# Kernel optimization log

Measured on AMD Instinct MI355X. Metric: run time of the kernel, lower is better.

The kernel has to match this reference:

```python
import jax, jax.numpy as jnp
import numpy as np

EMBED = 768
NHEAD = 12
HEAD_DIM = EMBED // NHEAD


def setup_inputs() -> dict:
    key = jax.random.key(0)
    ks = jax.random.split(key, 6)
    bs, seq = 4, 2048
    x = jax.random.normal(ks[0], (bs, seq, EMBED), dtype=jnp.float32)
    attmask = jax.random.randint(ks[1], (bs, seq), 0, 2, dtype=jnp.int32)
    # xavier-uniform-ish init for weights
    lim_qkv = float(np.sqrt(6.0 / (EMBED + 3 * EMBED)))
    W_qkv = jax.random.uniform(ks[2], (EMBED, 3 * EMBED), minval=-lim_qkv, maxval=lim_qkv, dtype=jnp.float32)
    b_qkv = jnp.zeros((3 * EMBED,), dtype=jnp.float32)
    lim_p = float(np.sqrt(6.0 / (EMBED + EMBED)))
    W_proj = jax.random.uniform(ks[3], (EMBED, EMBED), minval=-lim_p, maxval=lim_p, dtype=jnp.float32)
    b_proj = jnp.zeros((EMBED,), dtype=jnp.float32)
    return {"x": x, "attmask": attmask, "W_qkv": W_qkv, "b_qkv": b_qkv, "W_proj": W_proj, "b_proj": b_proj}


def reference(x, attmask, W_qkv, b_qkv, W_proj, b_proj):
    bs, seq, embed = x.shape
    qkv = x @ W_qkv + b_qkv                     # [bs, seq, 3*embed]
    q, k, v = jnp.split(qkv, 3, axis=-1)
    def to_heads(t):
        return t.reshape(bs, seq, NHEAD, HEAD_DIM).transpose(0, 2, 1, 3)  # [bs, h, seq, d]
    q, k, v = to_heads(q), to_heads(k), to_heads(v)
    scale = 1.0 / np.sqrt(HEAD_DIM).astype(np.float32)
    scores = jnp.einsum('bhqd,bhkd->bhqk', q, k) * scale  # [bs, h, seq, seq]
    mask = (attmask == 0)[:, None, None, :]               # [bs,1,1,seq]
    scores = jnp.where(mask, jnp.asarray(-10000.0, scores.dtype), scores)
    att = jax.nn.softmax(scores, axis=-1)                  # dropout p=0.0 -> identity
    y = jnp.einsum('bhqk,bhkd->bhqd', att, v)              # [bs, h, seq, d]
    y = y.transpose(0, 2, 1, 3).reshape(bs, seq, embed)
    return y @ W_proj + b_proj
```

## Files before the change

### kernel.cpp

```cpp
#include <hip/hip_runtime.h>

typedef unsigned short u16;
typedef unsigned int u32;
typedef __attribute__((ext_vector_type(8))) short short8;
typedef __attribute__((ext_vector_type(4))) short s16x4;
typedef __attribute__((ext_vector_type(4))) float f32x4;

__device__ __forceinline__ float b2f(u16 u) {
    union { u32 i; float f; } v; v.i = ((u32)u) << 16; return v.f;
}
__device__ __forceinline__ u16 f2b(float f) {
    union { u32 i; float f; } v; v.f = f;
    u32 u = v.i;
    return (u16)((u + 0x7FFFu + ((u >> 16) & 1u)) >> 16);
}
__device__ __forceinline__ f32x4 zero4() {
    f32x4 v; v[0] = 0.f; v[1] = 0.f; v[2] = 0.f; v[3] = 0.f; return v;
}
__device__ __forceinline__ u32 cvtpk(float lo, float hi) {
    u32 d;
    asm("v_cvt_pk_bf16_f32 %0, %1, %2" : "=v"(d) : "v"(lo), "v"(hi));
    return d;
}
__device__ __forceinline__ float fexp2(float x) {
#if __has_builtin(__builtin_amdgcn_exp2f)
    return __builtin_amdgcn_exp2f(x);
#else
    return __expf(x * 0.6931471805599453f);
#endif
}
__device__ __forceinline__ void gload16(const u16* g, u16* l) {
    __builtin_amdgcn_global_load_lds(
        (const __attribute__((address_space(1))) u32*)g,
        (__attribute__((address_space(3))) u32*)l, 16, 0, 0);
}

__global__ void convert_kernel(const float* __restrict__ src, u16* __restrict__ dst,
                               int n8) {
    const int stride = gridDim.x * blockDim.x;
    for (int i = blockIdx.x * blockDim.x + threadIdx.x; i < n8; i += stride) {
        const float* s = src + (size_t)i * 8;
        float4 a = ((const float4*)s)[0];
        float4 b = ((const float4*)s)[1];
        short8 o;
        o[0] = (short)f2b(a.x); o[1] = (short)f2b(a.y);
        o[2] = (short)f2b(a.z); o[3] = (short)f2b(a.w);
        o[4] = (short)f2b(b.x); o[5] = (short)f2b(b.y);
        o[6] = (short)f2b(b.z); o[7] = (short)f2b(b.w);
        ((short8*)dst)[i] = o;
    }
}

__global__ void tconvert_kernel(const float* __restrict__ src, u16* __restrict__ dst,
                                int K, int N) {
    __shared__ u16 T[64][72];
    const int n0 = blockIdx.x * 64, k0 = blockIdx.y * 64;
    const int tid = threadIdx.x;
    const int r = tid >> 3, cq = tid & 7;
#pragma unroll
    for (int half = 0; half < 2; half++) {
        const int k = k0 + half * 32 + r;
        const float* s = &src[(size_t)k * N + n0 + cq * 8];
        const float4 f0 = ((const float4*)s)[0];
        const float4 f1 = ((const float4*)s)[1];
        T[cq * 8 + 0][half * 32 + r] = f2b(f0.x);
        T[cq * 8 + 1][half * 32 + r] = f2b(f0.y);
        T[cq * 8 + 2][half * 32 + r] = f2b(f0.z);
        T[cq * 8 + 3][half * 32 + r] = f2b(f0.w);
        T[cq * 8 + 4][half * 32 + r] = f2b(f1.x);
        T[cq * 8 + 5][half * 32 + r] = f2b(f1.y);
        T[cq * 8 + 6][half * 32 + r] = f2b(f1.z);
        T[cq * 8 + 7][half * 32 + r] = f2b(f1.w);
    }
    __syncthreads();
#pragma unroll
    for (int half = 0; half < 2; half++) {
        const int n = half * 32 + r;
        short8 o = *(const short8*)&T[n][cq * 8];
        *(short8*)&dst[(size_t)(n0 + n) * K + k0 + cq * 8] = o;
    }
}

template <int MODE>
__global__ __launch_bounds__(256, 2) void gemm_bt_kernel(
    const u16* __restrict__ A, const u16* __restrict__ Bt,
    const float* __restrict__ bias,
    u16* __restrict__ O0, u16* __restrict__ O1, u16* __restrict__ O2,
    float* __restrict__ Of,
    int M, int N, int K)
{
    __shared__ u16 As[128 * 32];
    __shared__ u16 Bs[128 * 32];

    const int tid = threadIdx.x;
    const int nwgx = gridDim.x;
    const int nwg = nwgx * gridDim.y;
    int lin = blockIdx.y * nwgx + blockIdx.x;
    lin = (lin & 7) * (nwg >> 3) + (lin >> 3);
    const int m0 = (lin / nwgx) * 128, n0 = (lin % nwgx) * 128;
    const int lane = tid & 63, w = tid >> 6;
    const int quad = lane >> 4, c = lane & 15;
    const int wm = (w & 1) * 64, wn = (w >> 1) * 64;

    f32x4 acc[4][4];
#pragma unroll
    for (int i = 0; i < 4; i++)
#pragma unroll
        for (int j = 0; j < 4; j++) acc[i][j] = zero4();

    const int grow = w * 32 + (lane >> 2);
    const int gcol = (lane & 3) * 8;
    const size_t abase = (size_t)(m0 + grow) * K + gcol;
    const size_t bbase = (size_t)(n0 + grow) * K + gcol;
    u16* asl = &As[w * 1024];
    u16* bsl = &Bs[w * 1024];

    for (int k0 = 0; k0 < K; k0 += 32) {
        __syncthreads();
        gload16(A + abase + k0, asl);
        gload16(A + abase + (size_t)16 * K + k0, asl + 512);
        gload16(Bt + bbase + k0, bsl);
        gload16(Bt + bbase + (size_t)16 * K + k0, bsl + 512);
        asm volatile("s_waitcnt vmcnt(0)" ::: "memory");
        __syncthreads();

        short8 af[4], bfr[4];
#pragma unroll
        for (int mi = 0; mi < 4; mi++)
            af[mi] = *(const short8*)&As[(wm + mi * 16 + c) * 32 + quad * 8];
#pragma unroll
        for (int ni = 0; ni < 4; ni++)
            bfr[ni] = *(const short8*)&Bs[(wn + ni * 16 + c) * 32 + quad * 8];
#pragma unroll
        for (int mi = 0; mi < 4; mi++)
#pragma unroll
            for (int ni = 0; ni < 4; ni++)
                acc[mi][ni] = __builtin_amdgcn_mfma_f32_16x16x32_bf16(
                    af[mi], bfr[ni], acc[mi][ni], 0, 0, 0);
    }

#pragma unroll
    for (int ni = 0; ni < 4; ni++) {
        const int gc = n0 + wn + ni * 16 + c;
        const float bv = bias[gc];
        if (MODE == 0) {
            const int which = gc / 768;
            const int e = gc - which * 768;
            const int hh = e >> 6, d = e & 63;
            u16* op = (which == 0) ? O0 : (which == 1 ? O1 : O2);
#pragma unroll
            for (int mi = 0; mi < 4; mi++)
#pragma unroll
                for (int r = 0; r < 4; r++) {
                    const int gr = m0 + wm + mi * 16 + quad * 4 + r;
                    const int bb = gr >> 11, s = gr & 2047;
                    op[(((size_t)bb * 12 + hh) * 2048 + s) * 64 + d] =
                        f2b(acc[mi][ni][r] + bv);
                }
        } else {
#pragma unroll
            for (int mi = 0; mi < 4; mi++)
#pragma unroll
                for (int r = 0; r < 4; r++) {
                    const int gr = m0 + wm + mi * 16 + quad * 4 + r;
                    Of[(size_t)gr * N + gc] = acc[mi][ni][r] + bv;
                }
        }
    }
}

__global__ __launch_bounds__(256, 3) void attn_kernel(
    const u16* __restrict__ Q, const u16* __restrict__ Kv,
    const u16* __restrict__ Vv, const int* __restrict__ attmask,
    u16* __restrict__ Y)
{
    const int S = 2048, D = 64, NH = 12;
    __shared__ u16 Ks[64][72];
    __shared__ u16 Vs[64][68];
    __shared__ u16 Ps[4][2][16][72];
    __shared__ float msf[2048];

    const int tid = threadIdx.x;
    const int w = tid >> 6, lane = tid & 63;
    const int quad = lane >> 4, c = lane & 15;
    const int bh = blockIdx.x;
    const int qt = blockIdx.y;
    const int b = bh / NH, h = bh - b * NH;

    const u16* Qh = Q + (size_t)bh * S * D;
    const u16* Kh = Kv + (size_t)bh * S * D;
    const u16* Vh = Vv + (size_t)bh * S * D;
    const int q0 = qt * 128 + w * 16;

    short8 aq00 = *(const short8*)&Qh[(size_t)(q0 + c) * D + quad * 8];
    short8 aq01 = *(const short8*)&Qh[(size_t)(q0 + c) * D + 32 + quad * 8];
    short8 aq10 = *(const short8*)&Qh[(size_t)(q0 + 64 + c) * D + quad * 8];
    short8 aq11 = *(const short8*)&Qh[(size_t)(q0 + 64 + c) * D + 32 + quad * 8];

    for (int i = tid; i < S; i += 256)
        msf[i] = (attmask[b * S + i] == 0) ? -43282.0f : 0.0f;

    f32x4 o_acc[2][4];
#pragma unroll
    for (int g = 0; g < 2; g++)
#pragma unroll
        for (int i = 0; i < 4; i++) o_acc[g][i] = zero4();
    float l0 = 0.f, l1 = 0.f;

    const int kpos = tid >> 2, kd = (tid & 3) * 8;
    const int p2 = tid >> 3, vd = (tid & 7) * 8;

    short8 k0r = *(const short8*)&Kh[(size_t)kpos * D + kd];
    short8 k1r = *(const short8*)&Kh[(size_t)kpos * D + kd + 32];
    short8 v0r = *(const short8*)&Vh[(size_t)(2 * p2) * D + vd];
    short8 v1r = *(const short8*)&Vh[(size_t)(2 * p2 + 1) * D + vd];

    const float SC = 0.18033688f;

    for (int kt = 0; kt < S / 64; kt++) {
        asm volatile("" ::: "memory");
        __builtin_amdgcn_s_barrier();
        asm volatile("" ::: "memory");
        *(short8*)&Ks[kpos][kd] = k0r;
        *(short8*)&Ks[kpos][kd + 32] = k1r;
#pragma unroll
        for (int j = 0; j < 8; j++) {
            u32 pk = (u32)(u16)v0r[j] | ((u32)(u16)v1r[j] << 16);
            *(u32*)&Vs[vd + j][2 * p2] = pk;
        }
        if (kt + 1 < S / 64) {
            const int nb = (kt + 1) * 64;
            k0r = *(const short8*)&Kh[(size_t)(nb + kpos) * D + kd];
            k1r = *(const short8*)&Kh[(size_t)(nb + kpos) * D + kd + 32];
            v0r = *(const short8*)&Vh[(size_t)(nb + 2 * p2) * D + vd];
            v1r = *(const short8*)&Vh[(size_t)(nb + 2 * p2 + 1) * D + vd];
        }
        asm volatile("s_waitcnt lgkmcnt(0)" ::: "memory");
        __builtin_amdgcn_s_barrier();
        asm volatile("" ::: "memory");

        const int kbase = kt * 64;

        f32x4 s0[4], s1[4];
#pragma unroll
        for (int ni = 0; ni < 4; ni++) { s0[ni] = zero4(); s1[ni] = zero4(); }
        __builtin_amdgcn_s_setprio(1);
#pragma unroll
        for (int ni = 0; ni < 4; ni++) {
            short8 bk0 = *(const short8*)&Ks[ni * 16 + c][quad * 8];
            short8 bk1 = *(const short8*)&Ks[ni * 16 + c][32 + quad * 8];
            s0[ni] = __builtin_amdgcn_mfma_f32_16x16x32_bf16(bk0, aq00, s0[ni], 0, 0, 0);
            s0[ni] = __builtin_amdgcn_mfma_f32_16x16x32_bf16(bk1, aq01, s0[ni], 0, 0, 0);
            s1[ni] = __builtin_amdgcn_mfma_f32_16x16x32_bf16(bk0, aq10, s1[ni], 0, 0, 0);
            s1[ni] = __builtin_amdgcn_mfma_f32_16x16x32_bf16(bk1, aq11, s1[ni], 0, 0, 0);
        }
        __builtin_amdgcn_s_setprio(0);

#pragma unroll
        for (int ni = 0; ni < 4; ni++) {
            const f32x4 bias = *(const f32x4*)&msf[kbase + ni * 16 + quad * 4];
            {
                float p0 = fexp2(fmaf(s0[ni][0], SC, bias[0]));
                float p1 = fexp2(fmaf(s0[ni][1], SC, bias[1]));
                float p2f = fexp2(fmaf(s0[ni][2], SC, bias[2]));
                float p3 = fexp2(fmaf(s0[ni][3], SC, bias[3]));
                l0 += (p0 + p1) + (p2f + p3);
                uint2 pk;
                pk.x = cvtpk(p0, p1);
                pk.y = cvtpk(p2f, p3);
                *(uint2*)&Ps[w][0][c][ni * 16 + quad * 4] = pk;
            }
            {
                float p0 = fexp2(fmaf(s1[ni][0], SC, bias[0]));
                float p1 = fexp2(fmaf(s1[ni][1], SC, bias[1]));
                float p2f = fexp2(fmaf(s1[ni][2], SC, bias[2]));
                float p3 = fexp2(fmaf(s1[ni][3], SC, bias[3]));
                l1 += (p0 + p1) + (p2f + p3);
                uint2 pk;
                pk.x = cvtpk(p0, p1);
                pk.y = cvtpk(p2f, p3);
                *(uint2*)&Ps[w][1][c][ni * 16 + quad * 4] = pk;
            }
        }

        short8 ap00 = *(const short8*)&Ps[w][0][c][quad * 8];
        short8 ap01 = *(const short8*)&Ps[w][0][c][32 + quad * 8];
        short8 ap10 = *(const short8*)&Ps[w][1][c][quad * 8];
        short8 ap11 = *(const short8*)&Ps[w][1][c][32 + quad * 8];
        __builtin_amdgcn_s_setprio(1);
#pragma unroll
        for (int ni = 0; ni < 4; ni++) {
            union { short8 v8; s16x4 v4[2]; } u0, u1;
            u0.v4[0] = *(const s16x4*)&Vs[ni * 16 + c][quad * 8];
            u0.v4[1] = *(const s16x4*)&Vs[ni * 16 + c][quad * 8 + 4];
            u1.v4[0] = *(const s16x4*)&Vs[ni * 16 + c][32 + quad * 8];
            u1.v4[1] = *(const s16x4*)&Vs[ni * 16 + c][32 + quad * 8 + 4];
            o_acc[0][ni] = __builtin_amdgcn_mfma_f32_16x16x32_bf16(ap00, u0.v8, o_acc[0][ni], 0, 0, 0);
            o_acc[0][ni] = __builtin_amdgcn_mfma_f32_16x16x32_bf16(ap01, u1.v8, o_acc[0][ni], 0, 0, 0);
            o_acc[1][ni] = __builtin_amdgcn_mfma_f32_16x16x32_bf16(ap10, u0.v8, o_acc[1][ni], 0, 0, 0);
            o_acc[1][ni] = __builtin_amdgcn_mfma_f32_16x16x32_bf16(ap11, u1.v8, o_acc[1][ni], 0, 0, 0);
        }
        __builtin_amdgcn_s_setprio(0);
    }

    l0 += __shfl_xor(l0, 16);
    l0 += __shfl_xor(l0, 32);
    l1 += __shfl_xor(l1, 16);
    l1 += __shfl_xor(l1, 32);

    const size_t ybase = ((size_t)b * S) * 768 + h * 64;
#pragma unroll
    for (int r = 0; r < 4; r++) {
        const float lr0 = __shfl(l0, quad * 4 + r);
        const float lr1 = __shfl(l1, quad * 4 + r);
        const float inv0 = 1.f / fmaxf(lr0, 1e-30f);
        const float inv1 = 1.f / fmaxf(lr1, 1e-30f);
        const int srow0 = qt * 128 + w * 16 + quad * 4 + r;
        const int srow1 = srow0 + 64;
#pragma unroll
        for (int ni = 0; ni < 4; ni++) {
            Y[ybase + (size_t)srow0 * 768 + ni * 16 + c] = f2b(o_acc[0][ni][r] * inv0);
            Y[ybase + (size_t)srow1 * 768 + ni * 16 + c] = f2b(o_acc[1][ni][r] * inv1);
        }
    }
}

extern "C" void kernel_launch(void* const* d_in, const int* in_sizes, int n_in,
                              void* d_out, int out_size, void* d_ws, size_t ws_size,
                              hipStream_t stream) {
    const float* x     = (const float*)d_in[0];
    const int* attmask = (const int*)d_in[1];
    const float* Wqkv  = (const float*)d_in[2];
    const float* bqkv  = (const float*)d_in[3];
    const float* Wproj = (const float*)d_in[4];
    const float* bproj = (const float*)d_in[5];
    float* outf = (float*)d_out;

    u16* base = (u16*)d_ws;
    const size_t nx = 4ull * 2048 * 768;
    const size_t nwqkv = 768ull * 2304;
    const size_t nwproj = 768ull * 768;
    u16* xb     = base;
    u16* Wqkvb  = xb + nx;
    u16* Wprojb = Wqkvb + nwqkv;
    u16* Qb     = Wprojb + nwproj;
    const size_t headElems = 48ull * 2048 * 64;
    u16* Kb = Qb + headElems;
    u16* Vb = Kb + headElems;
    u16* Yb = Vb + headElems;

    {
        int n8 = (int)(nx / 8);
        int blocks = (n8 + 255) / 256;
        if (blocks > 1024) blocks = 1024;
        convert_kernel<<<blocks, 256, 0, stream>>>(x, xb, n8);
    }
    tconvert_kernel<<<dim3(2304 / 64, 768 / 64), 256, 0, stream>>>(Wqkv, Wqkvb, 768, 2304);
    tconvert_kernel<<<dim3(768 / 64, 768 / 64), 256, 0, stream>>>(Wproj, Wprojb, 768, 768);

    gemm_bt_kernel<0><<<dim3(18, 64), 256, 0, stream>>>(
        xb, Wqkvb, bqkv, Qb, Kb, Vb, nullptr, 8192, 2304, 768);
    attn_kernel<<<dim3(48, 16), 256, 0, stream>>>(Qb, Kb, Vb, attmask, Yb);
    gemm_bt_kernel<1><<<dim3(6, 64), 256, 0, stream>>>(
        Yb, Wprojb, bproj, nullptr, nullptr, nullptr, outf, 8192, 768, 768);
}
```

Baseline: 238.4 us.

## Merge conversion kernels into one launch and deepen GEMM K-tile with swizzled LDS

After: 227.8 us. 1.05x faster.

```diff
diff --git a/kernel.cpp b/kernel.cpp
--- a/kernel.cpp
+++ b/kernel.cpp
@@ -35,26 +35,11 @@
         (__attribute__((address_space(3))) u32*)l, 16, 0, 0);
 }
 
-__global__ void convert_kernel(const float* __restrict__ src, u16* __restrict__ dst,
-                               int n8) {
-    const int stride = gridDim.x * blockDim.x;
-    for (int i = blockIdx.x * blockDim.x + threadIdx.x; i < n8; i += stride) {
-        const float* s = src + (size_t)i * 8;
-        float4 a = ((const float4*)s)[0];
-        float4 b = ((const float4*)s)[1];
-        short8 o;
-        o[0] = (short)f2b(a.x); o[1] = (short)f2b(a.y);
-        o[2] = (short)f2b(a.z); o[3] = (short)f2b(a.w);
-        o[4] = (short)f2b(b.x); o[5] = (short)f2b(b.y);
-        o[6] = (short)f2b(b.z); o[7] = (short)f2b(b.w);
-        ((short8*)dst)[i] = o;
-    }
-}
-
-__global__ void tconvert_kernel(const float* __restrict__ src, u16* __restrict__ dst,
-                                int K, int N) {
+__device__ __forceinline__ void tconv_body(const float* __restrict__ src,
+                                           u16* __restrict__ dst,
+                                           int K, int N, int bx, int by) {
     __shared__ u16 T[64][72];
-    const int n0 = blockIdx.x * 64, k0 = blockIdx.y * 64;
+    const int n0 = bx * 64, k0 = by * 64;
     const int tid = threadIdx.x;
     const int r = tid >> 3, cq = tid & 7;
 #pragma unroll
@@ -81,6 +66,32 @@
     }
 }
 
+__global__ void prep_kernel(const float* __restrict__ x, u16* __restrict__ xb,
+                            const float* __restrict__ Wqkv, u16* __restrict__ Wqkvb,
+                            const float* __restrict__ Wproj, u16* __restrict__ Wprojb,
+                            int n8x) {
+    const int blk = blockIdx.x;
+    if (blk < 432) {
+        tconv_body(Wqkv, Wqkvb, 768, 2304, blk % 36, blk / 36);
+    } else if (blk < 576) {
+        const int id = blk - 432;
+        tconv_body(Wproj, Wprojb, 768, 768, id % 12, id / 12);
+    } else {
+        const int stride = (1152 - 576) * 256;
+        for (int i = (blk - 576) * 256 + threadIdx.x; i < n8x; i += stride) {
+            const float* s = x + (size_t)i * 8;
+            float4 a = ((const float4*)s)[0];
+            float4 b = ((const float4*)s)[1];
+            short8 o;
+            o[0] = (short)f2b(a.x); o[1] = (short)f2b(a.y);
+            o[2] = (short)f2b(a.z); o[3] = (short)f2b(a.w);
+            o[4] = (short)f2b(b.x); o[5] = (short)f2b(b.y);
+            o[6] = (short)f2b(b.z); o[7] = (short)f2b(b.w);
+            ((short8*)xb)[i] = o;
+        }
+    }
+}
+
 template <int MODE>
 __global__ __launch_bounds__(256, 2) void gemm_bt_kernel(
     const u16* __restrict__ A, const u16* __restrict__ Bt,
@@ -89,8 +100,8 @@
     float* __restrict__ Of,
     int M, int N, int K)
 {
-    __shared__ u16 As[128 * 32];
-    __shared__ u16 Bs[128 * 32];
+    __shared__ u16 As[128 * 64];
+    __shared__ u16 Bs[128 * 64];
 
     const int tid = threadIdx.x;
     const int nwgx = gridDim.x;
@@ -108,35 +119,47 @@
 #pragma unroll
         for (int j = 0; j < 4; j++) acc[i][j] = zero4();
 
-    const int grow = w * 32 + (lane >> 2);
-    const int gcol = (lane & 3) * 8;
-    const size_t abase = (size_t)(m0 + grow) * K + gcol;
-    const size_t bbase = (size_t)(n0 + grow) * K + gcol;
-    u16* asl = &As[w * 1024];
-    u16* bsl = &Bs[w * 1024];
-
-    for (int k0 = 0; k0 < K; k0 += 32) {
+    const int srow = lane >> 3;
+    const int scol = ((lane & 7) ^ ((srow & 1) << 2)) * 8;
+    const size_t abase = (size_t)(m0 + w * 32 + srow) * K + scol;
+    const size_t bbase = (size_t)(n0 + w * 32 + srow) * K + scol;
+    u16* asl = &As[w * 32 * 64];
+    u16* bsl = &Bs[w * 32 * 64];
+
+    const int cpar = (c & 1) << 2;
+
+    for (int k0 = 0; k0 < K; k0 += 64) {
         __syncthreads();
-        gload16(A + abase + k0, asl);
-        gload16(A + abase + (size_t)16 * K + k0, asl + 512);
-        gload16(Bt + bbase + k0, bsl);
-        gload16(Bt + bbase + (size_t)16 * K + k0, bsl + 512);
+#pragma unroll
+        for (int i = 0; i < 4; i++)
+            gload16(A + abase + (size_t)(i * 8) * K + k0, asl + i * 512);
+#pragma unroll
+        for (int i = 0; i < 4; i++)
+            gload16(Bt + bbase + (size_t)(i * 8) * K + k0, bsl + i * 512);
         asm volatile("s_waitcnt vmcnt(0)" ::: "memory");
         __syncthreads();
 
-        short8 af[4], bfr[4];
+        short8 af[4][2], bfr[4][2];
 #pragma unroll
         for (int mi = 0; mi < 4; mi++)
-            af[mi] = *(const short8*)&As[(wm + mi * 16 + c) * 32 + quad * 8];
+#pragma unroll
+            for (int kk = 0; kk < 2; kk++)
+                af[mi][kk] = *(const short8*)
+                    &As[(wm + mi * 16 + c) * 64 + (((kk * 4 + quad) ^ cpar) * 8)];
 #pragma unroll
         for (int ni = 0; ni < 4; ni++)
-            bfr[ni] = *(const short8*)&Bs[(wn + ni * 16 + c) * 32 + quad * 8];
-#pragma unroll
-        for (int mi = 0; mi < 4; mi++)
-#pragma unroll
-            for (int ni = 0; ni < 4; ni++)
-                acc[mi][ni] = __builtin_amdgcn_mfma_f32_16x16x32_bf16(
-                    af[mi], bfr[ni], acc[mi][ni], 0, 0, 0);
+#pragma unroll
+            for (int kk = 0; kk < 2; kk++)
+                bfr[ni][kk] = *(const short8*)
+                    &Bs[(wn + ni * 16 + c) * 64 + (((kk * 4 + quad) ^ cpar) * 8)];
+#pragma unroll
+        for (int kk = 0; kk < 2; kk++)
+#pragma unroll
+            for (int mi = 0; mi < 4; mi++)
+#pragma unroll
+                for (int ni = 0; ni < 4; ni++)
+                    acc[mi][ni] = __builtin_amdgcn_mfma_f32_16x16x32_bf16(
+                        af[mi][kk], bfr[ni][kk], acc[mi][ni], 0, 0, 0);
     }
 
 #pragma unroll
@@ -349,14 +372,8 @@
     u16* Vb = Kb + headElems;
     u16* Yb = Vb + headElems;
 
-    {
-        int n8 = (int)(nx / 8);
-        int blocks = (n8 + 255) / 256;
-        if (blocks > 1024) blocks = 1024;
-        convert_kernel<<<blocks, 256, 0, stream>>>(x, xb, n8);
-    }
-    tconvert_kernel<<<dim3(2304 / 64, 768 / 64), 256, 0, stream>>>(Wqkv, Wqkvb, 768, 2304);
-    tconvert_kernel<<<dim3(768 / 64, 768 / 64), 256, 0, stream>>>(Wproj, Wprojb, 768, 768);
+    prep_kernel<<<1152, 256, 0, stream>>>(x, xb, Wqkv, Wqkvb, Wproj, Wprojb,
+                                          (int)(nx / 8));
 
     gemm_bt_kernel<0><<<dim3(18, 64), 256, 0, stream>>>(
         xb, Wqkvb, bqkv, Qb, Kb, Vb, nullptr, 8192, 2304, 768);
```
